# Optimization experiments

Measured on AMD Instinct MI355X. Metric: run time of the kernel, lower is better.

Reference implementation:

```python
import jax, jax.numpy as jnp
import numpy as np

B, S, D, H = 4, 2048, 1024, 16
DK = D // H
NEG = -1e9


def setup_inputs() -> dict:
    key = jax.random.key(0)
    ks = jax.random.split(key, 11)
    s = 1.0 / np.sqrt(D)
    inp = {
        "query": jax.random.normal(ks[0], (B, S, D), jnp.float32),
        "key": jax.random.normal(ks[1], (B, S, D), jnp.float32),
        "value": jax.random.normal(ks[2], (B, S, D), jnp.float32),
        # causal mask, broadcastable to [B, H, S, S]; 0 -> masked
        "mask": jnp.tril(jnp.ones((S, S), dtype=bool))[None, None],
        # torch Linear weights: [out, in], y = x @ W.T + b
        "Wq": jax.random.uniform(ks[3], (D, D), jnp.float32, -s, s),
        "bq": jax.random.uniform(ks[4], (D,), jnp.float32, -s, s),
        "Wk": jax.random.uniform(ks[5], (D, D), jnp.float32, -s, s),
        "bk": jax.random.uniform(ks[6], (D,), jnp.float32, -s, s),
        "Wv": jax.random.uniform(ks[7], (D, D), jnp.float32, -s, s),
        "bv": jax.random.uniform(ks[8], (D,), jnp.float32, -s, s),
        "Wo": jax.random.uniform(ks[9], (D, D), jnp.float32, -s, s),
        "bo": jax.random.uniform(ks[10], (D,), jnp.float32, -s, s),
    }
    return inp


def reference(query, key, value, mask, Wq, bq, Wk, bk, Wv, bv, Wo, bo):
    def proj(x, W, b):
        y = jnp.einsum('bsd,ed->bse', x, W) + b          # torch Linear: x @ W.T + b
        return y.reshape(B, S, H, DK).transpose(0, 2, 1, 3)  # [B, H, S, DK]

    Q = proj(query, Wq, bq)
    K = proj(key, Wk, bk)
    V = proj(value, Wv, bv)

    scale = 1.0 / np.sqrt(DK)
    scores = jnp.einsum('bhqd,bhkd->bhqk', Q, K) * scale  # [B, H, S, S]
    scores = jnp.where(mask, scores, NEG)
    attn = jax.nn.softmax(scores, axis=-1)
    out = jnp.einsum('bhqk,bhkd->bhqd', attn, V)          # [B, H, S, DK]
    out = out.transpose(0, 2, 1, 3).reshape(B, S, D)
    return jnp.einsum('bsd,ed->bse', out, Wo) + bo
```

## Files before the change

kernel.cpp:

```cpp
#include <hip/hip_runtime.h>
#include <stdint.h>

typedef __attribute__((ext_vector_type(8))) short bf16x8;
typedef __attribute__((ext_vector_type(4))) short s16x4;
typedef __attribute__((ext_vector_type(4))) float f32x4;
typedef __attribute__((ext_vector_type(16))) float f32x16;

#define DEVI __device__ __forceinline__

constexpr int B_ = 4, S_ = 2048, D_ = 1024, H_ = 16, DK_ = 64;
constexpr int M_ = B_ * S_;

DEVI short f2bf(float f) {
  union { float f; uint32_t u; } x; x.f = f;
  uint32_t r = x.u + 0x7fffu + ((x.u >> 16) & 1u);
  return (short)(uint16_t)(r >> 16);
}
DEVI float exp2_hw(float x) {
  float r; asm("v_exp_f32 %0, %1" : "=v"(r) : "v"(x)); return r;
}
DEVI uint32_t cvtpk(float lo, float hi) {
  uint32_t r; asm("v_cvt_pk_bf16_f32 %0, %1, %2" : "=v"(r) : "v"(lo), "v"(hi));
  return r;
}
DEVI void gload16(const short* g, short* l) {
  __builtin_amdgcn_global_load_lds((const __attribute__((address_space(1))) uint32_t*)g,
                                   (__attribute__((address_space(3))) uint32_t*)l, 16, 0, 0);
}

__global__ __launch_bounds__(256) void cvt_f32_bf16(const float* __restrict__ in,
                                                    short* __restrict__ out, int n) {
  const int stride = gridDim.x * blockDim.x;
  const int ng = n >> 3;
  for (int g = blockIdx.x * blockDim.x + threadIdx.x; g < ng; g += stride) {
    const f32x4 a = *(const f32x4*)(in + (size_t)g * 8);
    const f32x4 b = *(const f32x4*)(in + (size_t)g * 8 + 4);
    bf16x8 o;
#pragma unroll
    for (int e = 0; e < 4; ++e) { o[e] = f2bf(a[e]); o[e + 4] = f2bf(b[e]); }
    *(bf16x8*)(out + (size_t)g * 8) = o;
  }
}

template <int MODE>
__global__ __launch_bounds__(256) void gemm_bt(const short* __restrict__ A,
                                               const short* __restrict__ Bw,
                                               const float* __restrict__ bias,
                                               void* __restrict__ Cout,
                                               int Kdim, int Ndim, float scale) {
  __shared__ short sA[2][128 * 32];
  __shared__ short sB[2][128 * 32];
  const int tid = threadIdx.x;
  const int wid = tid >> 6, lane = tid & 63;
  const int m0 = blockIdx.x * 128, n0 = blockIdx.y * 128;
  const int wm = wid >> 1, wn = wid & 1;

  f32x4 acc[4][4];
#pragma unroll
  for (int i = 0; i < 4; ++i)
#pragma unroll
    for (int j = 0; j < 4; ++j) acc[i][j] = (f32x4){0.f, 0.f, 0.f, 0.f};

  const int srow = wid * 32 + (lane >> 2);
  const int swzs = (srow & 3) ^ ((srow >> 2) & 3);
  const int scol = ((lane & 3) ^ swzs) * 8;
  const short* gA = A + (size_t)(m0 + srow) * Kdim + scol;
  const short* gB = Bw + (size_t)(n0 + srow) * Kdim + scol;

  auto STAGE = [&](int bi, int kt) {
    short* la = &sA[bi][(wid * 32) * 32];
    short* lb = &sB[bi][(wid * 32) * 32];
    gload16(gA + kt, la);
    gload16(gA + (size_t)16 * Kdim + kt, la + 16 * 32);
    gload16(gB + kt, lb);
    gload16(gB + (size_t)16 * Kdim + kt, lb + 16 * 32);
  };

  STAGE(0, 0);
  __syncthreads();
  int cur = 0;

  const int swzf = (lane & 3) ^ ((lane >> 2) & 3);
  const int cofs = (((lane >> 4) ^ swzf) << 3);

  for (int kt = 0; kt < Kdim; kt += 32) {
    if (kt + 32 < Kdim) STAGE(cur ^ 1, kt + 32);
    bf16x8 af[4], bfr[4];
#pragma unroll
    for (int mf = 0; mf < 4; ++mf)
      af[mf] = *(const bf16x8*)&sA[cur][(wm * 64 + mf * 16 + (lane & 15)) * 32 + cofs];
#pragma unroll
    for (int nf = 0; nf < 4; ++nf)
      bfr[nf] = *(const bf16x8*)&sB[cur][(wn * 64 + nf * 16 + (lane & 15)) * 32 + cofs];
#pragma unroll
    for (int mf = 0; mf < 4; ++mf)
#pragma unroll
      for (int nf = 0; nf < 4; ++nf)
        acc[mf][nf] = __builtin_amdgcn_mfma_f32_16x16x32_bf16(af[mf], bfr[nf], acc[mf][nf], 0, 0, 0);
    __syncthreads();
    cur ^= 1;
  }

#pragma unroll
  for (int mf = 0; mf < 4; ++mf) {
#pragma unroll
    for (int nf = 0; nf < 4; ++nf) {
      const int n = n0 + wn * 64 + nf * 16 + (lane & 15);
      const float bi = bias[n];
      if (MODE == 2) {
        const int m_base = m0 + wm * 64 + mf * 16 + ((lane >> 4) * 4);
        const int b = m_base >> 11, s0 = m_base & 2047;
        s16x4 pk;
#pragma unroll
        for (int r = 0; r < 4; ++r) pk[r] = f2bf(acc[mf][nf][r] + bi);
        *(s16x4*)((short*)Cout + ((size_t)(b * 1024 + n)) * 2048 + s0) = pk;
      } else {
#pragma unroll
        for (int r = 0; r < 4; ++r) {
          const int m = m0 + wm * 64 + mf * 16 + ((lane >> 4) * 4) + r;
          const float vv = (acc[mf][nf][r] + bi) * scale;
          if (MODE == 0)
            ((short*)Cout)[(size_t)m * Ndim + n] = f2bf(vv);
          else
            ((float*)Cout)[(size_t)m * Ndim + n] = vv;
        }
      }
    }
  }
}

__global__ __launch_bounds__(512, 4) void attn_fwd(const short* __restrict__ Qf,
                                                   const short* __restrict__ Kf,
                                                   const short* __restrict__ Vt,
                                                   short* __restrict__ AO) {
  __shared__ short sK[2][64 * 64];
  __shared__ short sV[2][64 * 64];

  const int tid = threadIdx.x, wid = tid >> 6, lane = tid & 63;
  const int h = lane >> 5, ql = lane & 31;
  const int cpx = gridDim.x >> 3;
  const int wg = ((int)blockIdx.x & 7) * cpx + ((int)blockIdx.x >> 3);
  const int bh = wg >> 3;
  const int pi = wg & 7;
  const int b = bh >> 4, hd = bh & 15;
  const int panel = (wid < 4) ? (15 - pi) : pi;
  const int qw = panel * 128 + (wid & 3) * 32;
  const int qg = qw + ql;
  const size_t rowbase = (size_t)b * S_ * D_ + (size_t)hd * DK_;
  const size_t vbase = (size_t)bh * 64 * S_;

  bf16x8 aQ[4];
  {
    const short* qp = Qf + rowbase + (size_t)qg * D_ + h * 8;
#pragma unroll
    for (int d = 0; d < 4; ++d) aQ[d] = *(const bf16x8*)(qp + d * 16);
  }

  f32x16 o0, o1;
#pragma unroll
  for (int i = 0; i < 16; ++i) { o0[i] = 0.f; o1[i] = 0.f; }
  float m_run = -1e30f, lsum = 0.f;

  const int srow8 = lane >> 3;
  const int schunk = ((lane & 7) ^ srow8) * 8;
  const short* gK = Kf + rowbase + (size_t)(wid * 8 + srow8) * D_ + schunk;
  const short* gV = Vt + vbase + (size_t)(wid * 8 + srow8) * S_ + schunk;

  auto STAGE = [&](int bufi, int kt) {
    gload16(gK + (size_t)kt * D_, &sK[bufi][(wid * 8) * 64]);
    gload16(gV + kt, &sV[bufi][(wid * 8) * 64]);
  };

  const int nt = 32 - 2 * pi;
  STAGE(0, 0);
  __syncthreads();
  int cur = 0;

  for (int t = 0; t < nt; ++t) {
    const int kt = t * 64;
    if (t + 1 < nt) STAGE(cur ^ 1, kt + 64);
    if (kt <= qw + 31) {
      const short* bK = &sK[cur][0];
      const short* bV = &sV[cur][0];
      f32x16 p0, p1;
#pragma unroll
      for (int i = 0; i < 16; ++i) { p0[i] = 0.f; p1[i] = 0.f; }
      __builtin_amdgcn_s_setprio(1);
#pragma unroll
      for (int d = 0; d < 4; ++d) {
        const int c = d * 2 + h;
        bf16x8 k0 = *(const bf16x8*)&bK[ql * 64 + ((c ^ (ql & 7)) << 3)];
        bf16x8 k1 = *(const bf16x8*)&bK[(32 + ql) * 64 + ((c ^ (ql & 7)) << 3)];
        p0 = __builtin_amdgcn_mfma_f32_32x32x16_bf16(k0, aQ[d], p0, 0, 0, 0);
        p1 = __builtin_amdgcn_mfma_f32_32x32x16_bf16(k1, aQ[d], p1, 0, 0, 0);
      }
      __builtin_amdgcn_s_setprio(0);
      if (kt + 63 > qw) {
        const int qk = qg - kt;
#pragma unroll
        for (int i = 0; i < 16; ++i) {
          const int k0i = 8 * (i >> 2) + 4 * h + (i & 3);
          if (k0i > qk) p0[i] = -1e30f;
          if (k0i + 32 > qk) p1[i] = -1e30f;
        }
      }
      float mx = fmaxf(p0[0], p1[0]);
#pragma unroll
      for (int i = 1; i < 16; ++i) mx = fmaxf(mx, fmaxf(p0[i], p1[i]));
      mx = fmaxf(mx, __shfl_xor(mx, 32));
      if (mx > m_run + 8.f) {
        const float corr = exp2_hw(m_run - mx);
        m_run = mx;
        lsum *= corr;
#pragma unroll
        for (int i = 0; i < 16; ++i) { o0[i] *= corr; o1[i] *= corr; }
      }
      float rs = 0.f;
#pragma unroll
      for (int i = 0; i < 16; ++i) {
        p0[i] = exp2_hw(p0[i] - m_run); rs += p0[i];
        p1[i] = exp2_hw(p1[i] - m_run); rs += p1[i];
      }
      rs += __shfl_xor(rs, 32);
      lsum += rs;
      uint32_t cj[8], dj[8];
#pragma unroll
      for (int j = 0; j < 4; ++j) {
        cj[j]     = cvtpk(p0[4 * j], p0[4 * j + 1]);
        dj[j]     = cvtpk(p0[4 * j + 2], p0[4 * j + 3]);
        cj[4 + j] = cvtpk(p1[4 * j], p1[4 * j + 1]);
        dj[4 + j] = cvtpk(p1[4 * j + 2], p1[4 * j + 3]);
      }
#pragma unroll
      for (int m = 0; m < 4; ++m) {
        const uint32_t pc = h ? cj[2 * m] : cj[2 * m + 1];
        const uint32_t pd = h ? dj[2 * m] : dj[2 * m + 1];
        const uint32_t rc = (uint32_t)__shfl_xor((int)pc, 32);
        const uint32_t rd = (uint32_t)__shfl_xor((int)pd, 32);
        union { uint32_t w[4]; bf16x8 v; } u;
        u.w[0] = h ? rc : cj[2 * m];
        u.w[1] = h ? rd : dj[2 * m];
        u.w[2] = h ? cj[2 * m + 1] : rc;
        u.w[3] = h ? dj[2 * m + 1] : rd;
        const int cv = m * 2 + h;
        bf16x8 v0 = *(const bf16x8*)&bV[ql * 64 + ((cv ^ (ql & 7)) << 3)];
        bf16x8 v1 = *(const bf16x8*)&bV[(32 + ql) * 64 + ((cv ^ (ql & 7)) << 3)];
        __builtin_amdgcn_s_setprio(1);
        o0 = __builtin_amdgcn_mfma_f32_32x32x16_bf16(v0, u.v, o0, 0, 0, 0);
        o1 = __builtin_amdgcn_mfma_f32_32x32x16_bf16(v1, u.v, o1, 0, 0, 0);
        __builtin_amdgcn_s_setprio(0);
      }
    }
    __syncthreads();
    cur ^= 1;
  }

  const float invl = 1.f / lsum;
  short* op = AO + rowbase + (size_t)qg * D_;
#pragma unroll
  for (int j = 0; j < 4; ++j) {
    s16x4 w0, w1;
#pragma unroll
    for (int r = 0; r < 4; ++r) {
      w0[r] = f2bf(o0[4 * j + r] * invl);
      w1[r] = f2bf(o1[4 * j + r] * invl);
    }
    *(s16x4*)(op + 8 * j + 4 * h) = w0;
    *(s16x4*)(op + 32 + 8 * j + 4 * h) = w1;
  }
}

extern "C" void kernel_launch(void* const* d_in, const int* in_sizes, int n_in,
                              void* d_out, int out_size, void* d_ws, size_t ws_size,
                              hipStream_t stream) {
  (void)in_sizes; (void)n_in; (void)out_size; (void)ws_size;
  const float* q  = (const float*)d_in[0];
  const float* k  = (const float*)d_in[1];
  const float* v  = (const float*)d_in[2];
  const float* Wq = (const float*)d_in[4];
  const float* bq = (const float*)d_in[5];
  const float* Wk = (const float*)d_in[6];
  const float* bk = (const float*)d_in[7];
  const float* Wv = (const float*)d_in[8];
  const float* bv = (const float*)d_in[9];
  const float* Wo = (const float*)d_in[10];
  const float* bo = (const float*)d_in[11];

  char* ws = (char*)d_ws;
  const size_t MB = 1ull << 20;
  short* wqb = (short*)(ws + 0 * MB);
  short* wkb = (short*)(ws + 2 * MB);
  short* wvb = (short*)(ws + 4 * MB);
  short* wob = (short*)(ws + 6 * MB);
  short* Qf  = (short*)(ws + 8 * MB);
  short* Kf  = (short*)(ws + 24 * MB);
  short* Vtb = (short*)(ws + 40 * MB);
  short* xq  = (short*)(ws + 56 * MB);
  short* xk  = (short*)(ws + 72 * MB);
  short* xv  = (short*)(ws + 88 * MB);
  short* AO  = xq;

  const int BSD = B_ * S_ * D_;
  cvt_f32_bf16<<<4096, 256, 0, stream>>>(q, xq, BSD);
  cvt_f32_bf16<<<4096, 256, 0, stream>>>(k, xk, BSD);
  cvt_f32_bf16<<<4096, 256, 0, stream>>>(v, xv, BSD);
  cvt_f32_bf16<<<512, 256, 0, stream>>>(Wq, wqb, D_ * D_);
  cvt_f32_bf16<<<512, 256, 0, stream>>>(Wk, wkb, D_ * D_);
  cvt_f32_bf16<<<512, 256, 0, stream>>>(Wv, wvb, D_ * D_);
  cvt_f32_bf16<<<512, 256, 0, stream>>>(Wo, wob, D_ * D_);

  dim3 gg(M_ / 128, D_ / 128);
  gemm_bt<0><<<gg, 256, 0, stream>>>(xq, wqb, bq, Qf, D_, D_, 0.125f * 1.4426950408889634f);
  gemm_bt<0><<<gg, 256, 0, stream>>>(xk, wkb, bk, Kf, D_, D_, 1.0f);
  gemm_bt<2><<<gg, 256, 0, stream>>>(xv, wvb, bv, Vtb, D_, D_, 1.0f);

  attn_fwd<<<dim3(512), 512, 0, stream>>>(Qf, Kf, Vtb, AO);

  gemm_bt<1><<<gg, 256, 0, stream>>>(AO, wob, bo, d_out, D_, D_, 1.0f);
}
```

Baseline: 213.4 us.

## Batch conversion launches and restructure attention inner loop with permlane swaps

```diff
diff --git a/kernel.cpp b/kernel.cpp
--- a/kernel.cpp
+++ b/kernel.cpp
@@ -5,6 +5,7 @@
 typedef __attribute__((ext_vector_type(4))) short s16x4;
 typedef __attribute__((ext_vector_type(4))) float f32x4;
 typedef __attribute__((ext_vector_type(16))) float f32x16;
+typedef __attribute__((ext_vector_type(2))) unsigned u32x2;
 
 #define DEVI __device__ __forceinline__
 
@@ -23,22 +24,49 @@
   uint32_t r; asm("v_cvt_pk_bf16_f32 %0, %1, %2" : "=v"(r) : "v"(lo), "v"(hi));
   return r;
 }
+#if __has_builtin(__builtin_amdgcn_permlane32_swap)
+DEVI void plswap(uint32_t& a, uint32_t& b) {
+  u32x2 r = __builtin_amdgcn_permlane32_swap(a, b, false, false);
+  a = r[0]; b = r[1];
+}
+#else
+DEVI void plswap(uint32_t& a, uint32_t& b) {
+  const int h = (threadIdx.x & 63) >> 5;
+  const uint32_t pa = (uint32_t)__shfl_xor((int)a, 32);
+  const uint32_t pb = (uint32_t)__shfl_xor((int)b, 32);
+  const uint32_t na = h ? pb : a;
+  const uint32_t nb = h ? b : pa;
+  a = na; b = nb;
+}
+#endif
 DEVI void gload16(const short* g, short* l) {
   __builtin_amdgcn_global_load_lds((const __attribute__((address_space(1))) uint32_t*)g,
                                    (__attribute__((address_space(3))) uint32_t*)l, 16, 0, 0);
 }
 
-__global__ __launch_bounds__(256) void cvt_f32_bf16(const float* __restrict__ in,
-                                                    short* __restrict__ out, int n) {
+template <int LOG2G>
+__global__ __launch_bounds__(256) void cvt3(const float* __restrict__ s0,
+                                            const float* __restrict__ s1,
+                                            const float* __restrict__ s2,
+                                            const float* __restrict__ s3,
+                                            short* __restrict__ d0,
+                                            short* __restrict__ d1,
+                                            short* __restrict__ d2,
+                                            short* __restrict__ d3,
+                                            int narr) {
   const int stride = gridDim.x * blockDim.x;
-  const int ng = n >> 3;
-  for (int g = blockIdx.x * blockDim.x + threadIdx.x; g < ng; g += stride) {
-    const f32x4 a = *(const f32x4*)(in + (size_t)g * 8);
-    const f32x4 b = *(const f32x4*)(in + (size_t)g * 8 + 4);
+  const int total = narr << LOG2G;
+  for (int g = blockIdx.x * blockDim.x + threadIdx.x; g < total; g += stride) {
+    const int a = g >> LOG2G;
+    const size_t off = (size_t)(g & ((1 << LOG2G) - 1)) * 8;
+    const float* src = (a == 0) ? s0 : (a == 1) ? s1 : (a == 2) ? s2 : s3;
+    short* dst = (a == 0) ? d0 : (a == 1) ? d1 : (a == 2) ? d2 : d3;
+    const f32x4 x = *(const f32x4*)(src + off);
+    const f32x4 y = *(const f32x4*)(src + off + 4);
     bf16x8 o;
 #pragma unroll
-    for (int e = 0; e < 4; ++e) { o[e] = f2bf(a[e]); o[e + 4] = f2bf(b[e]); }
-    *(bf16x8*)(out + (size_t)g * 8) = o;
+    for (int e = 0; e < 4; ++e) { o[e] = f2bf(x[e]); o[e + 4] = f2bf(y[e]); }
+    *(bf16x8*)(dst + off) = o;
   }
 }
 
@@ -176,25 +204,38 @@
   __syncthreads();
   int cur = 0;
 
+  const int swz = ((ql & 7) << 3);
+
   for (int t = 0; t < nt; ++t) {
     const int kt = t * 64;
     if (t + 1 < nt) STAGE(cur ^ 1, kt + 64);
     if (kt <= qw + 31) {
       const short* bK = &sK[cur][0];
       const short* bV = &sV[cur][0];
+      bf16x8 kf[8];
+#pragma unroll
+      for (int d = 0; d < 4; ++d) {
+        const int co = ((d * 2 + h) << 3) ^ swz;
+        kf[d]     = *(const bf16x8*)&bK[ql * 64 + co];
+        kf[4 + d] = *(const bf16x8*)&bK[(32 + ql) * 64 + co];
+      }
       f32x16 p0, p1;
 #pragma unroll
       for (int i = 0; i < 16; ++i) { p0[i] = 0.f; p1[i] = 0.f; }
       __builtin_amdgcn_s_setprio(1);
 #pragma unroll
       for (int d = 0; d < 4; ++d) {
-        const int c = d * 2 + h;
-        bf16x8 k0 = *(const bf16x8*)&bK[ql * 64 + ((c ^ (ql & 7)) << 3)];
-        bf16x8 k1 = *(const bf16x8*)&bK[(32 + ql) * 64 + ((c ^ (ql & 7)) << 3)];
-        p0 = __builtin_amdgcn_mfma_f32_32x32x16_bf16(k0, aQ[d], p0, 0, 0, 0);
-        p1 = __builtin_amdgcn_mfma_f32_32x32x16_bf16(k1, aQ[d], p1, 0, 0, 0);
+        p0 = __builtin_amdgcn_mfma_f32_32x32x16_bf16(kf[d], aQ[d], p0, 0, 0, 0);
+        p1 = __builtin_amdgcn_mfma_f32_32x32x16_bf16(kf[4 + d], aQ[d], p1, 0, 0, 0);
       }
       __builtin_amdgcn_s_setprio(0);
+      bf16x8 vf[8];
+#pragma unroll
+      for (int m = 0; m < 4; ++m) {
+        const int co = ((m * 2 + h) << 3) ^ swz;
+        vf[m]     = *(const bf16x8*)&bV[ql * 64 + co];
+        vf[4 + m] = *(const bf16x8*)&bV[(32 + ql) * 64 + co];
+      }
       if (kt + 63 > qw) {
         const int qk = qg - kt;
 #pragma unroll
@@ -204,25 +245,36 @@
           if (k0i + 32 > qk) p1[i] = -1e30f;
         }
       }
-      float mx = fmaxf(p0[0], p1[0]);
-#pragma unroll
-      for (int i = 1; i < 16; ++i) mx = fmaxf(mx, fmaxf(p0[i], p1[i]));
-      mx = fmaxf(mx, __shfl_xor(mx, 32));
-      if (mx > m_run + 8.f) {
-        const float corr = exp2_hw(m_run - mx);
-        m_run = mx;
+      float tr[8];
+#pragma unroll
+      for (int i = 0; i < 8; ++i)
+        tr[i] = fmaxf(fmaxf(p0[i], p0[i + 8]), fmaxf(p1[i], p1[i + 8]));
+#pragma unroll
+      for (int s = 4; s > 0; s >>= 1)
+#pragma unroll
+        for (int i = 0; i < s; ++i) tr[i] = fmaxf(tr[i], tr[i + s]);
+      float mx = fmaxf(tr[0], __shfl_xor(tr[0], 32));
+      if (__any(mx > m_run + 8.f)) {
+        const float mnew = fmaxf(m_run, mx);
+        const float corr = exp2_hw(m_run - mnew);
+        m_run = mnew;
         lsum *= corr;
 #pragma unroll
         for (int i = 0; i < 16; ++i) { o0[i] *= corr; o1[i] *= corr; }
       }
-      float rs = 0.f;
 #pragma unroll
       for (int i = 0; i < 16; ++i) {
-        p0[i] = exp2_hw(p0[i] - m_run); rs += p0[i];
-        p1[i] = exp2_hw(p1[i] - m_run); rs += p1[i];
-      }
-      rs += __shfl_xor(rs, 32);
-      lsum += rs;
+        p0[i] = exp2_hw(p0[i] - m_run);
+        p1[i] = exp2_hw(p1[i] - m_run);
+      }
+      float sr[8];
+#pragma unroll
+      for (int i = 0; i < 8; ++i) sr[i] = (p0[i] + p0[i + 8]) + (p1[i] + p1[i + 8]);
+#pragma unroll
+      for (int s = 4; s > 0; s >>= 1)
+#pragma unroll
+        for (int i = 0; i < s; ++i) sr[i] += sr[i + s];
+      lsum += sr[0] + __shfl_xor(sr[0], 32);
       uint32_t cj[8], dj[8];
 #pragma unroll
       for (int j = 0; j < 4; ++j) {
@@ -231,25 +283,19 @@
         cj[4 + j] = cvtpk(p1[4 * j], p1[4 * j + 1]);
         dj[4 + j] = cvtpk(p1[4 * j + 2], p1[4 * j + 3]);
       }
+      __builtin_amdgcn_s_setprio(1);
 #pragma unroll
       for (int m = 0; m < 4; ++m) {
-        const uint32_t pc = h ? cj[2 * m] : cj[2 * m + 1];
-        const uint32_t pd = h ? dj[2 * m] : dj[2 * m + 1];
-        const uint32_t rc = (uint32_t)__shfl_xor((int)pc, 32);
-        const uint32_t rd = (uint32_t)__shfl_xor((int)pd, 32);
+        uint32_t w0 = cj[2 * m], w2 = cj[2 * m + 1];
+        plswap(w0, w2);
+        uint32_t w1 = dj[2 * m], w3 = dj[2 * m + 1];
+        plswap(w1, w3);
         union { uint32_t w[4]; bf16x8 v; } u;
-        u.w[0] = h ? rc : cj[2 * m];
-        u.w[1] = h ? rd : dj[2 * m];
-        u.w[2] = h ? cj[2 * m + 1] : rc;
-        u.w[3] = h ? dj[2 * m + 1] : rd;
-        const int cv = m * 2 + h;
-        bf16x8 v0 = *(const bf16x8*)&bV[ql * 64 + ((cv ^ (ql & 7)) << 3)];
-        bf16x8 v1 = *(const bf16x8*)&bV[(32 + ql) * 64 + ((cv ^ (ql & 7)) << 3)];
-        __builtin_amdgcn_s_setprio(1);
-        o0 = __builtin_amdgcn_mfma_f32_32x32x16_bf16(v0, u.v, o0, 0, 0, 0);
-        o1 = __builtin_amdgcn_mfma_f32_32x32x16_bf16(v1, u.v, o1, 0, 0, 0);
-        __builtin_amdgcn_s_setprio(0);
-      }
+        u.w[0] = w0; u.w[1] = w1; u.w[2] = w2; u.w[3] = w3;
+        o0 = __builtin_amdgcn_mfma_f32_32x32x16_bf16(vf[m], u.v, o0, 0, 0, 0);
+        o1 = __builtin_amdgcn_mfma_f32_32x32x16_bf16(vf[4 + m], u.v, o1, 0, 0, 0);
+      }
+      __builtin_amdgcn_s_setprio(0);
     }
     __syncthreads();
     cur ^= 1;
@@ -300,14 +346,8 @@
   short* xv  = (short*)(ws + 88 * MB);
   short* AO  = xq;
 
-  const int BSD = B_ * S_ * D_;
-  cvt_f32_bf16<<<4096, 256, 0, stream>>>(q, xq, BSD);
-  cvt_f32_bf16<<<4096, 256, 0, stream>>>(k, xk, BSD);
-  cvt_f32_bf16<<<4096, 256, 0, stream>>>(v, xv, BSD);
-  cvt_f32_bf16<<<512, 256, 0, stream>>>(Wq, wqb, D_ * D_);
-  cvt_f32_bf16<<<512, 256, 0, stream>>>(Wk, wkb, D_ * D_);
-  cvt_f32_bf16<<<512, 256, 0, stream>>>(Wv, wvb, D_ * D_);
-  cvt_f32_bf16<<<512, 256, 0, stream>>>(Wo, wob, D_ * D_);
+  cvt3<20><<<2048, 256, 0, stream>>>(q, k, v, v, xq, xk, xv, xv, 3);
+  cvt3<17><<<1024, 256, 0, stream>>>(Wq, Wk, Wv, Wo, wqb, wkb, wvb, wob, 4);
 
   dim3 gg(M_ / 128, D_ / 128);
   gemm_bt<0><<<gg, 256, 0, stream>>>(xq, wqb, bq, Qf, D_, D_, 0.125f * 1.4426950408889634f);
```

New measurement: 227.3 us. 1.07x slower.
